# Kernel optimization log

Measured on AMD Instinct MI355X. Metric: run time of the kernel, lower is better.

The kernel has to match this reference:

```python
import jax, jax.numpy as jnp
import numpy as np

B, NPG, DEG, D, H, K, NHID, CB = 64, 512, 16, 128, 4, 5, 50, 512
N = B * NPG
E = N * DEG
TAU = 1.0
EPS = 1e-6
BN_SCALE = 1.0 / np.sqrt(1.0 + 1e-5)  # eval-mode BatchNorm, running mean=0 var=1


def _forward(x, edge_index, batch, emb, gin_W1, gin_b1, gin_W2, gin_b2, bn_gamma, bn_beta, part_W1, part_b1, part_W2, part_b2, Wq, Wk, Wv, Wo, gate_W1, gate_b1, gate_W2, gate_b2, codebook, cls_W1, cls_b1, cls_W2, cls_b2, cls_W3, cls_b3):
    # --- GIN stack: h_i <- MLP((1+eps)*h_i + sum_{j->i} h_j), eps=0 ---
    h = emb[x]  # [N, D]
    src, dst = edge_index[0], edge_index[1]
    n_layers = gin_W1.shape[0]
    for l in range(n_layers):
        agg = jax.ops.segment_sum(h[src], dst, num_segments=N)  # scatter-add neighbor messages
        z = h + agg
        z = jax.nn.relu(z @ gin_W1[l] + gin_b1[l]) @ gin_W2[l] + gin_b2[l]
        z = z * (BN_SCALE * bn_gamma[l]) + bn_beta[l]  # eval BN
        h = jax.nn.relu(z) if l < n_layers - 1 else z
    # --- to_dense_batch (equal-size graphs) + soft partitioner ---
    dense = h.reshape(B, NPG, D)
    cl = jax.nn.relu(dense @ part_W1 + part_b1) @ part_W2 + part_b2  # [B,NPG,K]
    S = jax.nn.softmax(cl / TAU, axis=-1)  # soft node->cluster assignment
    cf = jnp.einsum('bnk,bnd->bkd', S, dense) / (S.sum(1)[..., None] + EPS)
    # --- VQ codebook (l2 nearest neighbor, straight-through) ---
    flat = cf.reshape(-1, D)
    d2 = (flat * flat).sum(-1, keepdims=True) - 2.0 * flat @ codebook.T + (codebook * codebook).sum(-1)
    idx = jnp.argmin(d2, axis=-1)
    zq = cf + jax.lax.stop_gradient(codebook[idx].reshape(B, K, D) - cf)
    # --- scatter-mean graph pooling over batch vector ---
    residue = jax.ops.segment_sum(h, batch, num_segments=B) / NPG  # [B,D]
    # --- global cluster attention (4 heads), residue query vs cluster keys ---
    dh = D // H
    q = (residue @ Wq).reshape(B, H, dh)
    k = (zq @ Wk).reshape(B, K, H, dh)
    v = (zq @ Wv).reshape(B, K, H, dh)
    aw = jax.nn.softmax(jnp.einsum('bhd,bkhd->bhk', q, k) / np.sqrt(dh), axis=-1)
    att = jnp.einsum('bhk,bkhd->bhd', aw, v).reshape(B, D) @ Wo
    # --- feature-wise gated fusion ---
    cat = jnp.concatenate([residue, att], axis=-1)
    g = jax.nn.sigmoid(jax.nn.relu(cat @ gate_W1 + gate_b1) @ gate_W2 + gate_b2)
    fused = g * residue + (1.0 - g) * att
    # --- classifier MLP ---
    z1 = jax.nn.relu(fused @ cls_W1 + cls_b1)
    z2 = jax.nn.relu(z1 @ cls_W2 + cls_b2)
    return z2 @ cls_W3 + cls_b3


def setup_inputs():
    key = jax.random.key(0)
    ks = jax.random.split(key, 20)
    def lin(k, i, o):
        return jax.random.normal(k, (i, o), jnp.float32) / np.sqrt(i)
    x = jax.random.randint(ks[0], (N,), 0, 21, dtype=jnp.int32)
    srcn = jnp.repeat(jnp.arange(N, dtype=jnp.int32), DEG)
    dstn = (srcn // NPG) * NPG + jax.random.randint(ks[1], (E,), 0, NPG, dtype=jnp.int32)
    edge_index = jnp.stack([srcn, dstn])
    batch = jnp.repeat(jnp.arange(B, dtype=jnp.int32), NPG)
    return {
        'x': x, 'edge_index': edge_index, 'batch': batch,
        'emb': jax.random.normal(ks[2], (21, D), jnp.float32) * 0.02,
        'gin_W1': jax.random.normal(ks[3], (3, D, 2 * D), jnp.float32) / np.sqrt(D),
        'gin_b1': jnp.zeros((3, 2 * D), jnp.float32),
        'gin_W2': jax.random.normal(ks[4], (3, 2 * D, D), jnp.float32) / np.sqrt(2 * D),
        'gin_b2': jnp.zeros((3, D), jnp.float32),
        'bn_gamma': jnp.ones((3, D), jnp.float32),
        'bn_beta': jnp.zeros((3, D), jnp.float32),
        'part_W1': lin(ks[5], D, NHID), 'part_b1': jnp.zeros((NHID,), jnp.float32),
        'part_W2': lin(ks[6], NHID, K), 'part_b2': jnp.zeros((K,), jnp.float32),
        'Wq': lin(ks[7], D, D), 'Wk': lin(ks[8], D, D), 'Wv': lin(ks[9], D, D), 'Wo': lin(ks[10], D, D),
        'gate_W1': lin(ks[11], 2 * D, D // 2), 'gate_b1': jnp.zeros((D // 2,), jnp.float32),
        'gate_W2': lin(ks[12], D // 2, D), 'gate_b2': jnp.zeros((D,), jnp.float32),
        'codebook': jax.random.normal(ks[13], (CB, D), jnp.float32) * 0.1,
        'cls_W1': lin(ks[14], D, 4 * D), 'cls_b1': jnp.zeros((4 * D,), jnp.float32),
        'cls_W2': lin(ks[15], 4 * D, 2 * D), 'cls_b2': jnp.zeros((2 * D,), jnp.float32),
        'cls_W3': lin(ks[16], 2 * D, 2), 'cls_b3': jnp.zeros((2,), jnp.float32),
    }


def reference(x, edge_index, batch, emb, gin_W1, gin_b1, gin_W2, gin_b2, bn_gamma, bn_beta, part_W1, part_b1, part_W2, part_b2, Wq, Wk, Wv, Wo, gate_W1, gate_b1, gate_W2, gate_b2, codebook, cls_W1, cls_b1, cls_W2, cls_b2, cls_W3, cls_b3):
    return _forward(x, edge_index, batch, emb, gin_W1, gin_b1, gin_W2, gin_b2, bn_gamma, bn_beta, part_W1, part_b1, part_W2, part_b2, Wq, Wk, Wv, Wo, gate_W1, gate_b1, gate_W2, gate_b2, codebook, cls_W1, cls_b1, cls_W2, cls_b2, cls_W3, cls_b3)
```

## Files before the change

### kernel.cpp

```cpp
#include <hip/hip_runtime.h>

constexpr int B_    = 64;
constexpr int NPG_  = 512;
constexpr int D_    = 128;
constexpr int K_    = 5;
constexpr int NHID_ = 50;
constexpr int CB_   = 512;
constexpr int N_    = B_ * NPG_;
constexpr int E_    = N_ * 16;
constexpr float BN_SCALE_ = 0.99999500003749969f;
constexpr float EPS_ = 1e-6f;

typedef __attribute__((ext_vector_type(8))) short bf16x8_t;
typedef __attribute__((ext_vector_type(4))) float f32x4_t;

__device__ __forceinline__ unsigned short f2bf(float x) {
    unsigned int u = __float_as_uint(x);
    unsigned int r = (u + 0x7FFFu + ((u >> 16) & 1u)) >> 16;
    return (unsigned short)r;
}
__device__ __forceinline__ float bf2f(unsigned short b) {
    return __uint_as_float(((unsigned int)b) << 16);
}

__device__ __forceinline__ f32x4_t mfma3(bf16x8_t a0, bf16x8_t a1,
                                         bf16x8_t b0, bf16x8_t b1, f32x4_t acc) {
    acc = __builtin_amdgcn_mfma_f32_16x16x32_bf16(a1, b0, acc, 0, 0, 0);
    acc = __builtin_amdgcn_mfma_f32_16x16x32_bf16(a0, b1, acc, 0, 0, 0);
    acc = __builtin_amdgcn_mfma_f32_16x16x32_bf16(a0, b0, acc, 0, 0, 0);
    return acc;
}

__global__ void k_prep(const float* __restrict__ gw1, const float* __restrict__ gw2,
                       unsigned short* __restrict__ w1h, unsigned short* __restrict__ w1l,
                       unsigned short* __restrict__ w2h, unsigned short* __restrict__ w2l) {
    int e = blockIdx.x * 256 + threadIdx.x;
    int layer = e >> 16, rem = e & 65535;
    if (rem < 32768) {
        int k = rem >> 8, n = rem & 255;
        float v = gw1[layer * 32768 + rem];
        unsigned short h0 = f2bf(v);
        int o = layer * 32768 +
                ((((n >> 4) * 4 + (k >> 5)) * 64 + ((k >> 3) & 3) * 16 + (n & 15)) << 3) + (k & 7);
        w1h[o] = h0; w1l[o] = f2bf(v - bf2f(h0));
    } else {
        int rr = rem - 32768;
        int c = rr >> 7, n = rr & 127;
        float v = gw2[layer * 32768 + rr];
        unsigned short h0 = f2bf(v);
        int o = layer * 32768 +
                ((((n >> 4) * 8 + (c >> 5)) * 64 + ((c >> 3) & 3) * 16 + (n & 15)) << 3) + (c & 7);
        w2h[o] = h0; w2l[o] = f2bf(v - bf2f(h0));
    }
}

__global__ __launch_bounds__(512) void k_csr(const int* __restrict__ dst,
                                             int* __restrict__ rowptr,
                                             int* __restrict__ col) {
    __shared__ int cnt[512];
    __shared__ int sc[512];
    __shared__ short dstS[8192];
    int g = blockIdx.x, t = threadIdx.x;
    int base = g * 8192;
    cnt[t] = 0;
    __syncthreads();
    for (int i = t; i < 8192; i += 512) {
        int d = dst[base + i] & 511;
        dstS[i] = (short)d;
        atomicAdd(&cnt[d], 1);
    }
    __syncthreads();
    int c0 = cnt[t];
    sc[t] = c0;
    __syncthreads();
    for (int off = 1; off < 512; off <<= 1) {
        int v = sc[t];
        int add = (t >= off) ? sc[t - off] : 0;
        __syncthreads();
        sc[t] = v + add;
        __syncthreads();
    }
    int excl = sc[t] - c0;
    rowptr[g * 512 + t] = base + excl;
    cnt[t] = excl;
    if (g == 0 && t == 0) rowptr[N_] = E_;
    __syncthreads();
    for (int i = t; i < 8192; i += 512) {
        int d = dstS[i];
        int p = atomicAdd(&cnt[d], 1);
        col[base + p] = g * 512 + (i >> 4);
    }
}

constexpr int LDH = 264;
constexpr int COLCAP = 1024;
constexpr int LDA = 520;



__global__ __launch_bounds__(512, 8) void k_gin0(
    const int* __restrict__ rowptr, const int* __restrict__ col,
    const int* __restrict__ xIdx, const float* __restrict__ emb,
    const unsigned short* __restrict__ w1h, const unsigned short* __restrict__ w1l,
    const unsigned short* __restrict__ w2h, const unsigned short* __restrict__ w2l,
    const float* __restrict__ b1, const float* __restrict__ b2,
    const float* __restrict__ gamma, const float* __restrict__ beta,
    unsigned short* __restrict__ oFH, unsigned short* __restrict__ oFL) {
    __shared__ int colS[COLCAP];
    __shared__ unsigned short bufH[32 * LDH];
    __shared__ unsigned short bufL[32 * LDH];
    __shared__ float embS[21 * 128];
    __shared__ int xS[512];
    int i = blockIdx.x;
    int xcd = i & 7;
    int slot = i >> 3;
    int g = (slot >> 4) * 8 + xcd;
    int tile = slot & 15;
    int rowBase = g * 512 + tile * 32;
    int t = threadIdx.x;
    int w = t >> 6, l = t & 63;
    int l15 = l & 15, quad = l >> 4;
    int half = l >> 5, lane4 = l & 31;

    int ebase = rowptr[rowBase];
    int ecnt  = rowptr[rowBase + 32] - ebase;
    bool inLds = (ecnt <= COLCAP);
    if (inLds)
        for (int j = t; j < ecnt; j += 512) colS[j] = col[ebase + j];
    for (int j = t; j < 21 * 128; j += 512) embS[j] = emb[j];
    if (t < 512) xS[t] = xIdx[(rowBase & ~511) + t];
    __syncthreads();

    #pragma unroll
    for (int jj = 0; jj < 2; jj++) {
        int row = w * 4 + half * 2 + jj;
        int node = rowBase + row;
        int beg = rowptr[node], end = rowptr[node + 1];
        float4 a = *(const float4*)&embS[xS[node & 511] * 128 + lane4 * 4];
        for (int e = beg; e < end; e++) {
            int c = (inLds ? colS[e - ebase] : col[e]) & 511;
            float4 p = *(const float4*)&embS[xS[c] * 128 + lane4 * 4];
            a.x += p.x; a.y += p.y; a.z += p.z; a.w += p.w;
        }
        unsigned short h0 = f2bf(a.x), h1 = f2bf(a.y), h2s = f2bf(a.z), h3 = f2bf(a.w);
        uint2 hv, lv;
        hv.x = (unsigned)h0 | ((unsigned)h1 << 16);
        hv.y = (unsigned)h2s | ((unsigned)h3 << 16);
        lv.x = (unsigned)f2bf(a.x - bf2f(h0)) | ((unsigned)f2bf(a.y - bf2f(h1)) << 16);
        lv.y = (unsigned)f2bf(a.z - bf2f(h2s)) | ((unsigned)f2bf(a.w - bf2f(h3)) << 16);
        *(uint2*)&bufH[row * LDH + lane4 * 4] = hv;
        *(uint2*)&bufL[row * LDH + lane4 * 4] = lv;
    }
    __syncthreads();

    f32x4_t acc[2][2];
    #pragma unroll
    for (int nt = 0; nt < 2; nt++) {
        float bb = b1[w * 32 + nt * 16 + l15];
        acc[0][nt] = (f32x4_t){bb, bb, bb, bb};
        acc[1][nt] = (f32x4_t){bb, bb, bb, bb};
    }
    #pragma unroll
    for (int kk = 0; kk < 4; kk++) {
        bf16x8_t ah[2], al[2];
        #pragma unroll
        for (int mt = 0; mt < 2; mt++) {
            int addr = (mt * 16 + l15) * LDH + kk * 32 + quad * 8;
            ah[mt] = *(const bf16x8_t*)&bufH[addr];
            al[mt] = *(const bf16x8_t*)&bufL[addr];
        }
        #pragma unroll
        for (int nt = 0; nt < 2; nt++) {
            int n16 = w * 2 + nt;
            int ga = (((n16 * 4 + kk) * 64 + l) << 3);
            bf16x8_t bh = *(const bf16x8_t*)&w1h[ga];
            bf16x8_t bl = *(const bf16x8_t*)&w1l[ga];
            acc[0][nt] = mfma3(ah[0], al[0], bh, bl, acc[0][nt]);
            acc[1][nt] = mfma3(ah[1], al[1], bh, bl, acc[1][nt]);
        }
    }
    __syncthreads();
    #pragma unroll
    for (int mt = 0; mt < 2; mt++)
        #pragma unroll
        for (int nt = 0; nt < 2; nt++) {
            int colL = w * 32 + nt * 16 + l15;
            #pragma unroll
            for (int r = 0; r < 4; r++) {
                int row = mt * 16 + quad * 4 + r;
                float v = fmaxf(acc[mt][nt][r], 0.f);
                unsigned short h0 = f2bf(v);
                bufH[row * LDH + colL] = h0;
                bufL[row * LDH + colL] = f2bf(v - bf2f(h0));
            }
        }
    __syncthreads();

    f32x4_t acc2[2];
    {
        float bb = b2[w * 16 + l15];
        acc2[0] = (f32x4_t){bb, bb, bb, bb};
        acc2[1] = (f32x4_t){bb, bb, bb, bb};
    }
    #pragma unroll
    for (int kkG = 0; kkG < 8; kkG++) {
        bf16x8_t ah[2], al[2];
        #pragma unroll
        for (int mt = 0; mt < 2; mt++) {
            int addr = (mt * 16 + l15) * LDH + kkG * 32 + quad * 8;
            ah[mt] = *(const bf16x8_t*)&bufH[addr];
            al[mt] = *(const bf16x8_t*)&bufL[addr];
        }
        int ga = (((w * 8 + kkG) * 64 + l) << 3);
        bf16x8_t bh = *(const bf16x8_t*)&w2h[ga];
        bf16x8_t bl = *(const bf16x8_t*)&w2l[ga];
        acc2[0] = mfma3(ah[0], al[0], bh, bl, acc2[0]);
        acc2[1] = mfma3(ah[1], al[1], bh, bl, acc2[1]);
    }
    {
        int colC = w * 16 + l15;
        float gm = BN_SCALE_ * gamma[colC];
        float be = beta[colC];
        unsigned short* oH = oFH + (size_t)g * 65536;
        unsigned short* oL = oFL + (size_t)g * 65536;
        #pragma unroll
        for (int mt = 0; mt < 2; mt++) {
            int obase = (((w * 16 + tile) * 64) + (mt * 2 + (quad >> 1)) * 16 + l15) * 8 + (quad & 1) * 4;
            ushort4 vh, vl;
            #pragma unroll
            for (int r = 0; r < 4; r++) {
                float v = fmaxf(fmaf(acc2[mt][r], gm, be), 0.f);
                unsigned short hh = f2bf(v);
                unsigned short ll = f2bf(v - bf2f(hh));
                if (r == 0) { vh.x = hh; vl.x = ll; }
                else if (r == 1) { vh.y = hh; vl.y = ll; }
                else if (r == 2) { vh.z = hh; vl.z = ll; }
                else { vh.w = hh; vl.w = ll; }
            }
            *(ushort4*)&oH[obase] = vh;
            *(ushort4*)&oL[obase] = vl;
        }
    }
}

template<int FRAG_OUT>
__global__ __launch_bounds__(512, 4) void k_ginF(
    const unsigned short* __restrict__ hFH, const unsigned short* __restrict__ hFL,
    const int* __restrict__ rowptr, const int* __restrict__ col,
    const unsigned short* __restrict__ w1h, const unsigned short* __restrict__ w1l,
    const unsigned short* __restrict__ w2h, const unsigned short* __restrict__ w2l,
    const float* __restrict__ b1, const float* __restrict__ b2,
    const float* __restrict__ gamma, const float* __restrict__ beta,
    unsigned short* __restrict__ oFH, unsigned short* __restrict__ oFL,
    float* __restrict__ hOut) {
    __shared__ unsigned short A16[32 * LDA];
    __shared__ unsigned short bufH[32 * LDH];
    __shared__ unsigned short bufL[32 * LDH];
    int i = blockIdx.x;
    int xcd = i & 7;
    int slot = i >> 3;
    int g = (slot >> 4) * 8 + xcd;
    int tile = slot & 15;
    int rowBase = g * 512 + tile * 32;
    int t = threadIdx.x;
    int w = t >> 6, l = t & 63;
    int l15 = l & 15, quad = l >> 4;

    for (int j = t; j < 32 * (LDA / 2); j += 512) ((unsigned int*)A16)[j] = 0;
    __syncthreads();
    if (t < 32) {
        int node = rowBase + t;
        int beg = rowptr[node], end = rowptr[node + 1];
        unsigned short* Arow = &A16[t * LDA];
        for (int e = beg; e < end; e++) {
            int c = col[e] & 511;
            Arow[c] = f2bf(bf2f(Arow[c]) + 1.0f);
        }
        int selfc = (rowBase & 511) + t;
        Arow[selfc] = f2bf(bf2f(Arow[selfc]) + 1.0f);
    }
    __syncthreads();

    const unsigned short* gFH = hFH + (size_t)g * 65536;
    const unsigned short* gFL = hFL + (size_t)g * 65536;
    f32x4_t zacc[2];
    zacc[0] = (f32x4_t){0, 0, 0, 0};
    zacc[1] = (f32x4_t){0, 0, 0, 0};
    #pragma unroll
    for (int kc = 0; kc < 16; kc++) {
        int ga = (((w * 16 + kc) * 64 + l) << 3);
        bf16x8_t bh = *(const bf16x8_t*)&gFH[ga];
        bf16x8_t bl = *(const bf16x8_t*)&gFL[ga];
        #pragma unroll
        for (int mt = 0; mt < 2; mt++) {
            bf16x8_t a = *(const bf16x8_t*)&A16[(mt * 16 + l15) * LDA + kc * 32 + quad * 8];
            zacc[mt] = __builtin_amdgcn_mfma_f32_16x16x32_bf16(a, bh, zacc[mt], 0, 0, 0);
            zacc[mt] = __builtin_amdgcn_mfma_f32_16x16x32_bf16(a, bl, zacc[mt], 0, 0, 0);
        }
    }
    #pragma unroll
    for (int mt = 0; mt < 2; mt++)
        #pragma unroll
        for (int r = 0; r < 4; r++) {
            int row = mt * 16 + quad * 4 + r;
            int colL = w * 16 + l15;
            float v = zacc[mt][r];
            unsigned short h0 = f2bf(v);
            bufH[row * LDH + colL] = h0;
            bufL[row * LDH + colL] = f2bf(v - bf2f(h0));
        }
    __syncthreads();

    f32x4_t acc[2][2];
    #pragma unroll
    for (int nt = 0; nt < 2; nt++) {
        float bb = b1[w * 32 + nt * 16 + l15];
        acc[0][nt] = (f32x4_t){bb, bb, bb, bb};
        acc[1][nt] = (f32x4_t){bb, bb, bb, bb};
    }
    #pragma unroll
    for (int kk = 0; kk < 4; kk++) {
        bf16x8_t ah[2], al[2];
        #pragma unroll
        for (int mt = 0; mt < 2; mt++) {
            int addr = (mt * 16 + l15) * LDH + kk * 32 + quad * 8;
            ah[mt] = *(const bf16x8_t*)&bufH[addr];
            al[mt] = *(const bf16x8_t*)&bufL[addr];
        }
        #pragma unroll
        for (int nt = 0; nt < 2; nt++) {
            int n16 = w * 2 + nt;
            int ga = (((n16 * 4 + kk) * 64 + l) << 3);
            bf16x8_t bh = *(const bf16x8_t*)&w1h[ga];
            bf16x8_t bl = *(const bf16x8_t*)&w1l[ga];
            acc[0][nt] = mfma3(ah[0], al[0], bh, bl, acc[0][nt]);
            acc[1][nt] = mfma3(ah[1], al[1], bh, bl, acc[1][nt]);
        }
    }
    __syncthreads();
    #pragma unroll
    for (int mt = 0; mt < 2; mt++)
        #pragma unroll
        for (int nt = 0; nt < 2; nt++) {
            int colL = w * 32 + nt * 16 + l15;
            #pragma unroll
            for (int r = 0; r < 4; r++) {
                int row = mt * 16 + quad * 4 + r;
                float v = fmaxf(acc[mt][nt][r], 0.f);
                unsigned short h0 = f2bf(v);
                bufH[row * LDH + colL] = h0;
                bufL[row * LDH + colL] = f2bf(v - bf2f(h0));
            }
        }
    __syncthreads();

    f32x4_t acc2[2];
    {
        float bb = b2[w * 16 + l15];
        acc2[0] = (f32x4_t){bb, bb, bb, bb};
        acc2[1] = (f32x4_t){bb, bb, bb, bb};
    }
    #pragma unroll
    for (int kkG = 0; kkG < 8; kkG++) {
        bf16x8_t ah[2], al[2];
        #pragma unroll
        for (int mt = 0; mt < 2; mt++) {
            int addr = (mt * 16 + l15) * LDH + kkG * 32 + quad * 8;
            ah[mt] = *(const bf16x8_t*)&bufH[addr];
            al[mt] = *(const bf16x8_t*)&bufL[addr];
        }
        int ga = (((w * 8 + kkG) * 64 + l) << 3);
        bf16x8_t bh = *(const bf16x8_t*)&w2h[ga];
        bf16x8_t bl = *(const bf16x8_t*)&w2l[ga];
        acc2[0] = mfma3(ah[0], al[0], bh, bl, acc2[0]);
        acc2[1] = mfma3(ah[1], al[1], bh, bl, acc2[1]);
    }
    {
        int colC = w * 16 + l15;
        float gm = BN_SCALE_ * gamma[colC];
        float be = beta[colC];
        if constexpr (FRAG_OUT) {
            unsigned short* oH = oFH + (size_t)g * 65536;
            unsigned short* oL = oFL + (size_t)g * 65536;
            #pragma unroll
            for (int mt = 0; mt < 2; mt++) {
                int obase = (((w * 16 + tile) * 64) + (mt * 2 + (quad >> 1)) * 16 + l15) * 8 + (quad & 1) * 4;
                ushort4 vh, vl;
                #pragma unroll
                for (int r = 0; r < 4; r++) {
                    float v = fmaxf(fmaf(acc2[mt][r], gm, be), 0.f);
                    unsigned short hh = f2bf(v);
                    unsigned short ll = f2bf(v - bf2f(hh));
                    if (r == 0) { vh.x = hh; vl.x = ll; }
                    else if (r == 1) { vh.y = hh; vl.y = ll; }
                    else if (r == 2) { vh.z = hh; vl.z = ll; }
                    else { vh.w = hh; vl.w = ll; }
                }
                *(ushort4*)&oH[obase] = vh;
                *(ushort4*)&oL[obase] = vl;
            }
        } else {
            #pragma unroll
            for (int mt = 0; mt < 2; mt++)
                #pragma unroll
                for (int r = 0; r < 4; r++) {
                    int row = mt * 16 + quad * 4 + r;
                    float v = fmaf(acc2[mt][r], gm, be);
                    hOut[(size_t)(rowBase + row) * 128 + colC] = v;
                }
        }
    }
}

__global__ __launch_bounds__(256) void k_partcf(
    const float* __restrict__ h,
    const float* __restrict__ W1, const float* __restrict__ b1,
    const float* __restrict__ W2, const float* __restrict__ b2,
    float* __restrict__ pacc, float* __restrict__ pss, float* __restrict__ prs) {
    __shared__ float zt[64 * 128];
    __shared__ float ht[64 * 52];
    __shared__ float lt[64 * 5];
    __shared__ float red[128 * 6];
    __shared__ float ssred[10];
    int t = threadIdx.x;
    int blk = blockIdx.x;
    int base = blk * 64;
    #pragma unroll
    for (int i = 0; i < 32; i++) { int idx = t + i * 256; zt[idx] = h[(size_t)base * D_ + idx]; }
    __syncthreads();
    int tx = t & 63, ty = t >> 6, r0 = ty * 16;
    if (tx < NHID_) {
        float acc[16];
        float bb = b1[tx];
        #pragma unroll
        for (int r = 0; r < 16; r++) acc[r] = bb;
        for (int k = 0; k < 128; k++) {
            float w = W1[k * NHID_ + tx];
            #pragma unroll
            for (int r = 0; r < 16; r++) acc[r] = fmaf(zt[(r0 + r) * 128 + k], w, acc[r]);
        }
        #pragma unroll
        for (int r = 0; r < 16; r++) ht[(r0 + r) * 52 + tx] = fmaxf(acc[r], 0.f);
    }
    __syncthreads();
    if (tx < K_) {
        float acc[16];
        float bb = b2[tx];
        #pragma unroll
        for (int r = 0; r < 16; r++) acc[r] = bb;
        for (int c = 0; c < NHID_; c++) {
            float w = W2[c * K_ + tx];
            #pragma unroll
            for (int r = 0; r < 16; r++) acc[r] = fmaf(ht[(r0 + r) * 52 + c], w, acc[r]);
        }
        #pragma unroll
        for (int r = 0; r < 16; r++) lt[(r0 + r) * 5 + tx] = acc[r];
    }
    __syncthreads();
    if (t < 64) {
        float l0 = lt[t*5], l1 = lt[t*5+1], l2 = lt[t*5+2], l3 = lt[t*5+3], l4 = lt[t*5+4];
        float m = fmaxf(fmaxf(fmaxf(l0, l1), fmaxf(l2, l3)), l4);
        float e0 = expf(l0 - m), e1 = expf(l1 - m), e2 = expf(l2 - m),
              e3 = expf(l3 - m), e4 = expf(l4 - m);
        float inv = 1.0f / (e0 + e1 + e2 + e3 + e4);
        lt[t*5]   = e0*inv; lt[t*5+1] = e1*inv; lt[t*5+2] = e2*inv;
        lt[t*5+3] = e3*inv; lt[t*5+4] = e4*inv;
    }
    __syncthreads();
    int d = t & 127, grp = t >> 7;
    float acc[5] = {0,0,0,0,0}, ssum[5] = {0,0,0,0,0}, rs = 0;
    #pragma unroll 4
    for (int i = 0; i < 32; i++) {
        int nl = grp * 32 + i;
        float hv = zt[nl * 128 + d];
        rs += hv;
        #pragma unroll
        for (int k = 0; k < 5; k++) {
            float sv = lt[nl * 5 + k];
            acc[k] = fmaf(sv, hv, acc[k]);
            ssum[k] += sv;
        }
    }
    if (grp == 1) {
        #pragma unroll
        for (int k = 0; k < 5; k++) red[d * 6 + k] = acc[k];
        red[d * 6 + 5] = rs;
    }
    if (d == 0) {
        #pragma unroll
        for (int k = 0; k < 5; k++) ssred[grp * 5 + k] = ssum[k];
    }
    __syncthreads();
    if (grp == 0) {
        #pragma unroll
        for (int k = 0; k < 5; k++) {
            acc[k] += red[d * 6 + k];
            pacc[((size_t)blk * 5 + k) * 128 + d] = acc[k];
        }
        rs += red[d * 6 + 5];
        prs[blk * 128 + d] = rs;
        if (d < 5) pss[blk * 5 + d] = ssred[d] + ssred[5 + d];
    }
}

__global__ __launch_bounds__(1024) void k_tail(
    const float* __restrict__ pacc, const float* __restrict__ pss,
    const float* __restrict__ prs, const float* __restrict__ cbk,
    const float* __restrict__ Wq, const float* __restrict__ Wk,
    const float* __restrict__ Wv, const float* __restrict__ Wo,
    const float* __restrict__ gW1, const float* __restrict__ gb1,
    const float* __restrict__ gW2, const float* __restrict__ gb2,
    const float* __restrict__ cW1, const float* __restrict__ cb1,
    const float* __restrict__ cW2, const float* __restrict__ cb2,
    const float* __restrict__ cW3, const float* __restrict__ cb3,
    float* __restrict__ out) {
    __shared__ float cfS[5 * 128];
    __shared__ float zqS[5 * 128];
    __shared__ float catS[256];
    __shared__ float qS[128];
    __shared__ float kS[5 * 128];
    __shared__ float vS[5 * 128];
    __shared__ float awS[20];
    __shared__ float att1S[128];
    __shared__ float attP[4][128];
    __shared__ float g1P[8][64];
    __shared__ float g1S[64];
    __shared__ float g2P[4][128];
    __shared__ float fusedS[128];
    __shared__ float z1P[2][512];
    __shared__ float z1S[512];
    __shared__ float z2P[4][256];
    __shared__ float bd5[5][512];
    __shared__ int   bi5[5][512];
    __shared__ int   idxS[5];
    __shared__ float red[8];

    int g = blockIdx.x, t = threadIdx.x;

    if (t < 768) {
        int c = t >> 7, d = t & 127;
        if (c == 5) {
            float rs = 0;
            #pragma unroll
            for (int ch = 0; ch < 8; ch++) rs += prs[(g * 8 + ch) * 128 + d];
            catS[d] = rs * (1.0f / 512.0f);
        } else {
            float acc = 0, ss = 0;
            #pragma unroll
            for (int ch = 0; ch < 8; ch++) {
                int blk = g * 8 + ch;
                acc += pacc[((size_t)blk * 5 + c) * 128 + d];
                ss  += pss[blk * 5 + c];
            }
            cfS[c * 128 + d] = acc / (ss + EPS_);
        }
    }
    __syncthreads();

    if (t < 512) {
        const float4* cj = (const float4*)(cbk + (size_t)t * 128);
        float d2[5] = {0, 0, 0, 0, 0};
        #pragma unroll 8
        for (int q4 = 0; q4 < 32; q4++) {
            float4 c4 = cj[q4];
            #pragma unroll
            for (int k = 0; k < 5; k++) {
                float4 f4 = ((const float4*)(cfS + k * 128))[q4];
                float dx = f4.x - c4.x, dy = f4.y - c4.y;
                float dz = f4.z - c4.z, dw = f4.w - c4.w;
                d2[k] = fmaf(dx, dx, d2[k]); d2[k] = fmaf(dy, dy, d2[k]);
                d2[k] = fmaf(dz, dz, d2[k]); d2[k] = fmaf(dw, dw, d2[k]);
            }
        }
        #pragma unroll
        for (int k = 0; k < 5; k++) { bd5[k][t] = d2[k]; bi5[k][t] = t; }
    }
    __syncthreads();
    for (int s = 256; s > 0; s >>= 1) {
        if (t < s) {
            #pragma unroll
            for (int k = 0; k < 5; k++) {
                float bo = bd5[k][t + s]; int io = bi5[k][t + s];
                if (bo < bd5[k][t] || (bo == bd5[k][t] && io < bi5[k][t])) {
                    bd5[k][t] = bo; bi5[k][t] = io;
                }
            }
        }
        __syncthreads();
    }
    if (t < 5) idxS[t] = bi5[t][0];
    __syncthreads();
    if (t < 640) zqS[t] = cbk[(size_t)idxS[t >> 7] * 128 + (t & 127)];
    __syncthreads();

    for (int o = t; o < 1408; o += 1024) {
        const float* Arow; const float* W; int dcol;
        if (o < 128)      { Arow = catS;                     W = Wq; dcol = o; }
        else if (o < 768) { Arow = &zqS[((o - 128) >> 7) * 128]; W = Wk; dcol = (o - 128) & 127; }
        else              { Arow = &zqS[((o - 768) >> 7) * 128]; W = Wv; dcol = (o - 768) & 127; }
        float acc = 0;
        for (int kk = 0; kk < 128; kk++) acc = fmaf(Arow[kk], W[kk * 128 + dcol], acc);
        if (o < 128)      qS[o] = acc;
        else if (o < 768) kS[o - 128] = acc;
        else              vS[o - 768] = acc;
    }
    __syncthreads();

    if (t < 20) {
        int hh = t / 5, j = t % 5;
        float s = 0;
        #pragma unroll
        for (int d2 = 0; d2 < 32; d2++)
            s = fmaf(qS[hh * 32 + d2], kS[j * 128 + hh * 32 + d2], s);
        awS[t] = s * 0.17677669529663687f;
    }
    __syncthreads();
    if (t < 4) {
        float m = -1e30f;
        for (int j = 0; j < 5; j++) m = fmaxf(m, awS[t * 5 + j]);
        float e[5], sum = 0;
        for (int j = 0; j < 5; j++) { e[j] = expf(awS[t * 5 + j] - m); sum += e[j]; }
        for (int j = 0; j < 5; j++) awS[t * 5 + j] = e[j] / sum;
    }
    __syncthreads();
    if (t < 128) {
        int hh = t >> 5;
        float a = 0;
        #pragma unroll
        for (int j = 0; j < 5; j++) a = fmaf(awS[hh * 5 + j], vS[j * 128 + t], a);
        att1S[t] = a;
    }
    __syncthreads();
    if (t < 512) {
        int o = t & 127, kq = t >> 7;
        float a = 0;
        #pragma unroll 8
        for (int i = 0; i < 32; i++) {
            int kk = kq * 32 + i;
            a = fmaf(att1S[kk], Wo[kk * 128 + o], a);
        }
        attP[kq][o] = a;
    }
    __syncthreads();
    if (t < 128) catS[128 + t] = attP[0][t] + attP[1][t] + attP[2][t] + attP[3][t];
    __syncthreads();

    if (t < 512) {
        int o = t & 63, kq = t >> 6;
        float a = 0;
        #pragma unroll 8
        for (int i = 0; i < 32; i++) {
            int kk = kq * 32 + i;
            a = fmaf(catS[kk], gW1[kk * 64 + o], a);
        }
        g1P[kq][o] = a;
    }
    __syncthreads();
    if (t < 64) {
        float a = gb1[t];
        #pragma unroll
        for (int q = 0; q < 8; q++) a += g1P[q][t];
        g1S[t] = fmaxf(a, 0.f);
    }
    __syncthreads();
    if (t < 512) {
        int o = t & 127, kq = t >> 7;
        float a = 0;
        #pragma unroll 8
        for (int i = 0; i < 16; i++) {
            int kk = kq * 16 + i;
            a = fmaf(g1S[kk], gW2[kk * 128 + o], a);
        }
        g2P[kq][o] = a;
    }
    __syncthreads();
    if (t < 128) {
        float a = gb2[t] + g2P[0][t] + g2P[1][t] + g2P[2][t] + g2P[3][t];
        float gv = 1.f / (1.f + expf(-a));
        fusedS[t] = gv * catS[t] + (1.f - gv) * catS[128 + t];
    }
    __syncthreads();

    {
        int o = t & 511, kq = t >> 9;
        float a = 0;
        #pragma unroll 8
        for (int i = 0; i < 64; i++) {
            int kk = kq * 64 + i;
            a = fmaf(fusedS[kk], cW1[kk * 512 + o], a);
        }
        z1P[kq][o] = a;
    }
    __syncthreads();
    if (t < 512) z1S[t] = fmaxf(z1P[0][t] + z1P[1][t] + cb1[t], 0.f);
    __syncthreads();
    {
        int o = t & 255, kq = t >> 8;
        float a = 0;
        #pragma unroll 8
        for (int i = 0; i < 128; i++) {
            int kk = kq * 128 + i;
            a = fmaf(z1S[kk], cW2[kk * 256 + o], a);
        }
        z2P[kq][o] = a;
    }
    __syncthreads();
    if (t < 256) {
        float zv = fmaxf(z2P[0][t] + z2P[1][t] + z2P[2][t] + z2P[3][t] + cb2[t], 0.f);
        float p0 = zv * cW3[t * 2];
        float p1 = zv * cW3[t * 2 + 1];
        #pragma unroll
        for (int off = 32; off > 0; off >>= 1) {
            p0 += __shfl_down(p0, off, 64);
            p1 += __shfl_down(p1, off, 64);
        }
        int wv = t >> 6;
        if ((t & 63) == 0) { red[wv * 2] = p0; red[wv * 2 + 1] = p1; }
    }
    __syncthreads();
    if (t < 2)
        out[g * 2 + t] = cb3[t] + red[t] + red[2 + t] + red[4 + t] + red[6 + t];
}

extern "C" void kernel_launch(void* const* d_in, const int* in_sizes, int n_in,
                              void* d_out, int out_size, void* d_ws, size_t ws_size,
                              hipStream_t stream) {
    const int*   x          = (const int*)d_in[0];
    const int*   edge_index = (const int*)d_in[1];
    const float* emb      = (const float*)d_in[3];
    const float* gin_W1   = (const float*)d_in[4];
    const float* gin_b1   = (const float*)d_in[5];
    const float* gin_W2   = (const float*)d_in[6];
    const float* gin_b2   = (const float*)d_in[7];
    const float* bn_gamma = (const float*)d_in[8];
    const float* bn_beta  = (const float*)d_in[9];
    const float* part_W1  = (const float*)d_in[10];
    const float* part_b1  = (const float*)d_in[11];
    const float* part_W2  = (const float*)d_in[12];
    const float* part_b2  = (const float*)d_in[13];
    const float* Wq       = (const float*)d_in[14];
    const float* Wk       = (const float*)d_in[15];
    const float* Wv       = (const float*)d_in[16];
    const float* Wo       = (const float*)d_in[17];
    const float* gate_W1  = (const float*)d_in[18];
    const float* gate_b1  = (const float*)d_in[19];
    const float* gate_W2  = (const float*)d_in[20];
    const float* gate_b2  = (const float*)d_in[21];
    const float* codebook = (const float*)d_in[22];
    const float* cls_W1   = (const float*)d_in[23];
    const float* cls_b1   = (const float*)d_in[24];
    const float* cls_W2   = (const float*)d_in[25];
    const float* cls_b2   = (const float*)d_in[26];
    const float* cls_W3   = (const float*)d_in[27];
    const float* cls_b3   = (const float*)d_in[28];

    const int* dstp = edge_index + E_;

    char* w = (char*)d_ws;
    float* hB = (float*)w;  w += (size_t)N_ * D_ * 4;
    int* rowptr = (int*)w;  w += (size_t)(N_ + 4) * 4;
    int* col    = (int*)w;  w += (size_t)E_ * 4;
    unsigned short* w1h = (unsigned short*)w;  w += (size_t)3 * 32768 * 2;
    unsigned short* w1l = (unsigned short*)w;  w += (size_t)3 * 32768 * 2;
    unsigned short* w2h = (unsigned short*)w;  w += (size_t)3 * 32768 * 2;
    unsigned short* w2l = (unsigned short*)w;  w += (size_t)3 * 32768 * 2;
    unsigned short* fragAH = (unsigned short*)w;  w += (size_t)B_ * 65536 * 2;
    unsigned short* fragAL = (unsigned short*)w;  w += (size_t)B_ * 65536 * 2;
    unsigned short* fragBH = (unsigned short*)w;  w += (size_t)B_ * 65536 * 2;
    unsigned short* fragBL = (unsigned short*)w;  w += (size_t)B_ * 65536 * 2;
    float* pacc = (float*)w;  w += (size_t)512 * 5 * 128 * 4;
    float* pss  = (float*)w;  w += (size_t)512 * 5 * 4;
    float* prs  = (float*)w;  w += (size_t)512 * 128 * 4;

    k_prep<<<768, 256, 0, stream>>>(gin_W1, gin_W2, w1h, w1l, w2h, w2l);
    k_csr <<<64, 512, 0, stream>>>(dstp, rowptr, col);

    k_gin0<<<1024, 512, 0, stream>>>(
        rowptr, col, x, emb,
        w1h, w1l, w2h, w2l,
        gin_b1, gin_b2, bn_gamma, bn_beta,
        fragAH, fragAL);
    k_ginF<1><<<1024, 512, 0, stream>>>(
        fragAH, fragAL, rowptr, col,
        w1h + 32768, w1l + 32768, w2h + 32768, w2l + 32768,
        gin_b1 + 256, gin_b2 + 128, bn_gamma + 128, bn_beta + 128,
        fragBH, fragBL, nullptr);
    k_ginF<0><<<1024, 512, 0, stream>>>(
        fragBH, fragBL, rowptr, col,
        w1h + 65536, w1l + 65536, w2h + 65536, w2l + 65536,
        gin_b1 + 512, gin_b2 + 256, bn_gamma + 256, bn_beta + 256,
        nullptr, nullptr, hB);

    k_partcf<<<512, 256, 0, stream>>>(hB, part_W1, part_b1, part_W2, part_b2,
                                      pacc, pss, prs);
    k_tail<<<B_, 1024, 0, stream>>>(pacc, pss, prs, codebook,
                                    Wq, Wk, Wv, Wo,
                                    gate_W1, gate_b1, gate_W2, gate_b2,
                                    cls_W1, cls_b1, cls_W2, cls_b2, cls_W3, cls_b3,
                                    (float*)d_out);
}
```

Baseline: 284.1 us.

## Alias GIN LDS buffers for higher occupancy and batch classifier MLP across graphs

In k_ginF, the adjacency tile and the hi/lo split buffers now share one LDS arena, with an extra barrier between uses. The tile's edge column indices are staged into LDS, and launch bounds go from 4 to 8 blocks per CU so more blocks can be resident. The classifier MLP moves out of the per-graph tail kernel into two batched kernels that load each weight slice once for all 64 graphs instead of once per graph. This costs two extra launches plus atomic accumulation into the output, and the output is first seeded with the bias.

```diff
diff --git a/kernel.cpp b/kernel.cpp
--- a/kernel.cpp
+++ b/kernel.cpp
@@ -95,7 +95,6 @@
 constexpr int LDH = 264;
 constexpr int COLCAP = 1024;
 constexpr int LDA = 520;
-
 
 
 __global__ __launch_bounds__(512, 8) void k_gin0(
@@ -244,7 +243,7 @@
 }
 
 template<int FRAG_OUT>
-__global__ __launch_bounds__(512, 4) void k_ginF(
+__global__ __launch_bounds__(512, 8) void k_ginF(
     const unsigned short* __restrict__ hFH, const unsigned short* __restrict__ hFL,
     const int* __restrict__ rowptr, const int* __restrict__ col,
     const unsigned short* __restrict__ w1h, const unsigned short* __restrict__ w1l,
@@ -253,9 +252,11 @@
     const float* __restrict__ gamma, const float* __restrict__ beta,
     unsigned short* __restrict__ oFH, unsigned short* __restrict__ oFL,
     float* __restrict__ hOut) {
-    __shared__ unsigned short A16[32 * LDA];
-    __shared__ unsigned short bufH[32 * LDH];
-    __shared__ unsigned short bufL[32 * LDH];
+    __shared__ int colS[COLCAP];
+    __shared__ __align__(16) char arena[33792];
+    unsigned short* A16  = (unsigned short*)arena;
+    unsigned short* bufH = (unsigned short*)arena;
+    unsigned short* bufL = (unsigned short*)(arena + 16896);
     int i = blockIdx.x;
     int xcd = i & 7;
     int slot = i >> 3;
@@ -267,16 +268,22 @@
     int l15 = l & 15, quad = l >> 4;
 
     for (int j = t; j < 32 * (LDA / 2); j += 512) ((unsigned int*)A16)[j] = 0;
-    __syncthreads();
+    int ebase = rowptr[rowBase];
+    int ecnt  = rowptr[rowBase + 32] - ebase;
+    bool inLds = (ecnt <= COLCAP);
+    if (inLds)
+        for (int j = t; j < ecnt; j += 512) colS[j] = col[ebase + j];
+    __syncthreads();
+
     if (t < 32) {
         int node = rowBase + t;
         int beg = rowptr[node], end = rowptr[node + 1];
         unsigned short* Arow = &A16[t * LDA];
         for (int e = beg; e < end; e++) {
-            int c = col[e] & 511;
+            int c = (inLds ? colS[e - ebase] : col[e]) & 511;
             Arow[c] = f2bf(bf2f(Arow[c]) + 1.0f);
         }
-        int selfc = (rowBase & 511) + t;
+        int selfc = tile * 32 + t;
         Arow[selfc] = f2bf(bf2f(Arow[selfc]) + 1.0f);
     }
     __syncthreads();
@@ -298,6 +305,8 @@
             zacc[mt] = __builtin_amdgcn_mfma_f32_16x16x32_bf16(a, bl, zacc[mt], 0, 0, 0);
         }
     }
+    __syncthreads();
+
     #pragma unroll
     for (int mt = 0; mt < 2; mt++)
         #pragma unroll
@@ -503,17 +512,15 @@
     }
 }
 
-__global__ __launch_bounds__(1024) void k_tail(
+__global__ __launch_bounds__(1024) void k_tail1(
     const float* __restrict__ pacc, const float* __restrict__ pss,
     const float* __restrict__ prs, const float* __restrict__ cbk,
     const float* __restrict__ Wq, const float* __restrict__ Wk,
     const float* __restrict__ Wv, const float* __restrict__ Wo,
     const float* __restrict__ gW1, const float* __restrict__ gb1,
     const float* __restrict__ gW2, const float* __restrict__ gb2,
-    const float* __restrict__ cW1, const float* __restrict__ cb1,
-    const float* __restrict__ cW2, const float* __restrict__ cb2,
-    const float* __restrict__ cW3, const float* __restrict__ cb3,
-    float* __restrict__ out) {
+    const float* __restrict__ cb3,
+    float* __restrict__ fusedG, float* __restrict__ out) {
     __shared__ float cfS[5 * 128];
     __shared__ float zqS[5 * 128];
     __shared__ float catS[256];
@@ -526,14 +533,9 @@
     __shared__ float g1P[8][64];
     __shared__ float g1S[64];
     __shared__ float g2P[4][128];
-    __shared__ float fusedS[128];
-    __shared__ float z1P[2][512];
-    __shared__ float z1S[512];
-    __shared__ float z2P[4][256];
     __shared__ float bd5[5][512];
     __shared__ int   bi5[5][512];
     __shared__ int   idxS[5];
-    __shared__ float red[8];
 
     int g = blockIdx.x, t = threadIdx.x;
 
@@ -555,6 +557,7 @@
             cfS[c * 128 + d] = acc / (ss + EPS_);
         }
     }
+    if (t >= 768 && t < 770) out[g * 2 + (t - 768)] = cb3[t - 768];
     __syncthreads();
 
     if (t < 512) {
@@ -677,49 +680,73 @@
     if (t < 128) {
         float a = gb2[t] + g2P[0][t] + g2P[1][t] + g2P[2][t] + g2P[3][t];
         float gv = 1.f / (1.f + expf(-a));
-        fusedS[t] = gv * catS[t] + (1.f - gv) * catS[128 + t];
-    }
-    __syncthreads();
-
-    {
-        int o = t & 511, kq = t >> 9;
-        float a = 0;
-        #pragma unroll 8
-        for (int i = 0; i < 64; i++) {
-            int kk = kq * 64 + i;
-            a = fmaf(fusedS[kk], cW1[kk * 512 + o], a);
-        }
-        z1P[kq][o] = a;
-    }
-    __syncthreads();
-    if (t < 512) z1S[t] = fmaxf(z1P[0][t] + z1P[1][t] + cb1[t], 0.f);
-    __syncthreads();
-    {
-        int o = t & 255, kq = t >> 8;
-        float a = 0;
-        #pragma unroll 8
-        for (int i = 0; i < 128; i++) {
-            int kk = kq * 128 + i;
-            a = fmaf(z1S[kk], cW2[kk * 256 + o], a);
-        }
-        z2P[kq][o] = a;
-    }
-    __syncthreads();
-    if (t < 256) {
-        float zv = fmaxf(z2P[0][t] + z2P[1][t] + z2P[2][t] + z2P[3][t] + cb2[t], 0.f);
-        float p0 = zv * cW3[t * 2];
-        float p1 = zv * cW3[t * 2 + 1];
-        #pragma unroll
-        for (int off = 32; off > 0; off >>= 1) {
-            p0 += __shfl_down(p0, off, 64);
-            p1 += __shfl_down(p1, off, 64);
-        }
-        int wv = t >> 6;
-        if ((t & 63) == 0) { red[wv * 2] = p0; red[wv * 2 + 1] = p1; }
-    }
-    __syncthreads();
-    if (t < 2)
-        out[g * 2 + t] = cb3[t] + red[t] + red[2 + t] + red[4 + t] + red[6 + t];
+        fusedG[g * 128 + t] = gv * catS[t] + (1.f - gv) * catS[128 + t];
+    }
+}
+
+__global__ __launch_bounds__(512) void k_cls1(
+    const float* __restrict__ fusedG, const float* __restrict__ cW1,
+    const float* __restrict__ cb1, float* __restrict__ z1G) {
+    __shared__ float fS[64 * 128];
+    __shared__ float wS[128 * 32];
+    int b = blockIdx.x, t = threadIdx.x;
+    for (int i = t; i < 2048; i += 512) ((float4*)fS)[i] = ((const float4*)fusedG)[i];
+    for (int i = t; i < 1024; i += 512) {
+        int k = i >> 3, c4 = (i & 7) * 4;
+        *(float4*)&wS[k * 32 + c4] = *(const float4*)&cW1[k * 512 + b * 32 + c4];
+    }
+    __syncthreads();
+    int c = t & 31, gs = t >> 5;
+    float bb = cb1[b * 32 + c];
+    float acc[4] = {bb, bb, bb, bb};
+    for (int k = 0; k < 128; k++) {
+        float wv = wS[k * 32 + c];
+        #pragma unroll
+        for (int gi = 0; gi < 4; gi++)
+            acc[gi] = fmaf(fS[(gs * 4 + gi) * 128 + k], wv, acc[gi]);
+    }
+    #pragma unroll
+    for (int gi = 0; gi < 4; gi++)
+        z1G[(gs * 4 + gi) * 512 + b * 32 + c] = fmaxf(acc[gi], 0.f);
+}
+
+__global__ __launch_bounds__(512) void k_cls2(
+    const float* __restrict__ z1G, const float* __restrict__ cW2,
+    const float* __restrict__ cb2, const float* __restrict__ cW3,
+    float* __restrict__ out) {
+    __shared__ float wS[512 * 16];
+    __shared__ float z1S[32 * 512];
+    int b = blockIdx.x, t = threadIdx.x;
+    for (int i = t; i < 2048; i += 512) {
+        int k = i >> 2, c4 = (i & 3) * 4;
+        *(float4*)&wS[k * 16 + c4] = *(const float4*)&cW2[k * 256 + b * 16 + c4];
+    }
+    int c = t & 15, gIn = t >> 4;
+    int cz = b * 16 + c;
+    float w3a = cW3[cz * 2], w3b = cW3[cz * 2 + 1];
+    float bb = cb2[cz];
+    for (int ch = 0; ch < 2; ch++) {
+        __syncthreads();
+        for (int i = t; i < 4096; i += 512)
+            ((float4*)z1S)[i] = ((const float4*)(z1G + (size_t)ch * 32 * 512))[i];
+        __syncthreads();
+        float acc = bb;
+        #pragma unroll 4
+        for (int k = 0; k < 512; k++)
+            acc = fmaf(z1S[gIn * 512 + k], wS[k * 16 + c], acc);
+        float zv = fmaxf(acc, 0.f);
+        float p0 = zv * w3a, p1 = zv * w3b;
+        #pragma unroll
+        for (int off = 8; off > 0; off >>= 1) {
+            p0 += __shfl_down(p0, off, 16);
+            p1 += __shfl_down(p1, off, 16);
+        }
+        if (c == 0) {
+            int g = ch * 32 + gIn;
+            atomicAdd(&out[g * 2], p0);
+            atomicAdd(&out[g * 2 + 1], p1);
+        }
+    }
 }
 
 extern "C" void kernel_launch(void* const* d_in, const int* in_sizes, int n_in,
@@ -771,6 +798,8 @@
     float* pacc = (float*)w;  w += (size_t)512 * 5 * 128 * 4;
     float* pss  = (float*)w;  w += (size_t)512 * 5 * 4;
     float* prs  = (float*)w;  w += (size_t)512 * 128 * 4;
+    float* fusedG = (float*)w;  w += (size_t)B_ * 128 * 4;
+    float* z1G    = (float*)w;  w += (size_t)B_ * 512 * 4;
 
     k_prep<<<768, 256, 0, stream>>>(gin_W1, gin_W2, w1h, w1l, w2h, w2l);
     k_csr <<<64, 512, 0, stream>>>(dstp, rowptr, col);
@@ -793,9 +822,10 @@
 
     k_partcf<<<512, 256, 0, stream>>>(hB, part_W1, part_b1, part_W2, part_b2,
                                       pacc, pss, prs);
-    k_tail<<<B_, 1024, 0, stream>>>(pacc, pss, prs, codebook,
-                                    Wq, Wk, Wv, Wo,
-                                    gate_W1, gate_b1, gate_W2, gate_b2,
-                                    cls_W1, cls_b1, cls_W2, cls_b2, cls_W3, cls_b3,
-                                    (float*)d_out);
-}
+    k_tail1<<<B_, 1024, 0, stream>>>(pacc, pss, prs, codebook,
+                                     Wq, Wk, Wv, Wo,
+                                     gate_W1, gate_b1, gate_W2, gate_b2,
+                                     cls_b3, fusedG, (float*)d_out);
+    k_cls1<<<16, 512, 0, stream>>>(fusedG, cls_W1, cls_b1, z1G);
+    k_cls2<<<16, 512, 0, stream>>>(z1G, cls_W2, cls_b2, cls_W3, (float*)d_out);
+}
```

Result: slower. 299.3 us (+5.4%).
